# Performance work log

Hardware: AMD Instinct MI355X
Metric: run time of the kernel (lower is better)

The kernel has to match this reference:

```python
import jax, jax.numpy as jnp
import numpy as np

B, L, D, NLAYERS, MAX_NODES, DEG = 32, 512, 768, 3, 128, 8


def _build_graph():
    rng = np.random.default_rng(0)
    per = rng.integers(-32, 33, size=B // 2)
    sizes = np.concatenate([96 + per, 96 - per]).astype(np.int64)  # sum = 96*B = 3072, each in [64,128]
    N = int(sizes.sum())
    offs = np.concatenate([[0], np.cumsum(sizes)])
    batch = np.repeat(np.arange(B), sizes).astype(np.int64)
    pad_idx = np.zeros((B, MAX_NODES), np.int64)
    pad_mask = np.zeros((B, MAX_NODES), bool)
    src, dst = [], []
    for b in range(B):
        n = int(sizes[b])
        pad_idx[b, :n] = np.arange(offs[b], offs[b] + n)
        pad_mask[b, :n] = True
        src.append(rng.integers(offs[b], offs[b] + n, n * DEG))
        dst.append(rng.integers(offs[b], offs[b] + n, n * DEG))
    return N, batch, pad_idx, pad_mask, np.concatenate(src), np.concatenate(dst)


def setup_inputs() -> dict:
    N, batch, pad_idx, pad_mask, esrc, edst = _build_graph()
    key = jax.random.key(0)
    ks = jax.random.split(key, 8)
    s = 1.0 / np.sqrt(D)
    return {
        "x": jax.random.normal(ks[0], (N, D), jnp.float32),
        "text": jax.random.normal(ks[1], (B, L, D), jnp.float32),
        "batch_ent1_d_mask": jnp.ones((B, 1), jnp.float32),
        "batch_ent1_g_mask": jnp.ones((B, 1), jnp.float32),
        "gnn_ws": jax.random.normal(ks[2], (NLAYERS, D, D), jnp.float32) * s,
        "gnn_wn": jax.random.normal(ks[3], (NLAYERS, D, D), jnp.float32) * s,
        "gnn_b": jnp.zeros((NLAYERS, D), jnp.float32),
        "atom_w": jax.random.normal(ks[4], (D, D), jnp.float32) * s,
        "atom_b": jnp.zeros((D,), jnp.float32),
        "rand_emb": jax.random.normal(ks[5], (1, D), jnp.float32),
        "batch": jnp.asarray(batch),
        "pad_idx": jnp.asarray(pad_idx),
        "pad_mask": jnp.asarray(pad_mask),
        "edge_src": jnp.asarray(esrc),
        "edge_dst": jnp.asarray(edst),
    }


def reference(x, text, batch_ent1_d_mask, batch_ent1_g_mask, gnn_ws, gnn_wn, gnn_b,
              atom_w, atom_b, rand_emb, batch, pad_idx, pad_mask, edge_src, edge_dst):
    N = x.shape[0]
    E = edge_src.shape[0]
    maskf = pad_mask.astype(x.dtype)            # [B, M]
    n_per = maskf.sum(axis=1)                   # [B] num real nodes per graph
    # edge-neighbor mean counts (constants w.r.t. x)
    cnt = jax.ops.segment_sum(jnp.ones((E,), x.dtype), edge_dst, num_segments=N)
    inv_cnt = 1.0 / jnp.maximum(cnt, 1.0)
    cms = []
    for i in range(NLAYERS):
        # MoleGraphConv stand-in: mean neighbor aggregation + self transform
        msg = jax.ops.segment_sum(x[edge_src], edge_dst, num_segments=N) * inv_cnt[:, None]
        x = jax.nn.relu(x @ gnn_ws[i] + msg @ gnn_wn[i] + gnn_b[i])
        # ragged gather into padded [B, M, D]
        xp = x[pad_idx] * maskf[..., None]
        # graph -> text cross attention (softmax over text tokens; no mask needed)
        g2t = jax.nn.softmax(jnp.einsum('bmd,bld->bml', xp, text), axis=-1)
        g2t_out = jnp.einsum('bml,bld->bmd', g2t, text)            # [B, M, D]
        # text -> graph cross attention (mask padded nodes)
        t2g_logits = jnp.einsum('bld,bmd->blm', text, xp)
        t2g_logits = jnp.where(pad_mask[:, None, :], t2g_logits, jnp.float32(-1e9))
        t2g = jax.nn.softmax(t2g_logits, axis=-1)
        t2g_out = jnp.einsum('blm,bmd->bld', t2g, xp)              # [B, L, D]
        # mean over concatenated rows [n_i + L] per graph (pool_type=2)
        pooled = ((g2t_out * maskf[..., None]).sum(axis=1) + t2g_out.sum(axis=1)) \
                 / (n_per + jnp.float32(L))[:, None]
        cms.append(pooled)
    out_cms = jnp.mean(jnp.stack(cms, axis=1), axis=1)              # mean over layers
    out_t = text[:, 0, :]
    # scatter-mean of final node features per graph
    gsum = jax.ops.segment_sum(x, batch, num_segments=B)
    gcnt = jax.ops.segment_sum(jnp.ones((N,), x.dtype), batch, num_segments=B)
    xg = gsum / jnp.maximum(gcnt, 1.0)[:, None]
    # dropout is a no-op in eval mode
    out_g = jnp.tanh(xg @ atom_w + atom_b)
    z = rand_emb[0]
    dg = batch_ent1_d_mask * batch_ent1_g_mask
    return jnp.concatenate([
        out_t * batch_ent1_d_mask + (1 - batch_ent1_d_mask) * z,
        out_g * batch_ent1_g_mask + (1 - batch_ent1_g_mask) * z,
        out_cms * dg + (1 - dg) * z,
    ], axis=-1)
```

## Files before the change

kernel.cpp:

```cpp
#include <hip/hip_runtime.h>

#define D 768
#define B 32
#define L 512
#define M 128
#define NNODES 3072
#define NEDGES 24576

using bf16x8 = __attribute__((ext_vector_type(8))) short;
using f32x4  = __attribute__((ext_vector_type(4))) float;

__device__ __forceinline__ float bf2f(unsigned short u) {
  union { unsigned int i; float f; } v; v.i = ((unsigned int)u) << 16; return v.f;
}
__device__ __forceinline__ unsigned short f2bf(float f) {
  union { float f; unsigned int i; } v; v.f = f;
  unsigned int x = v.i;
  return (unsigned short)((x + 0x7FFFu + ((x >> 16) & 1u)) >> 16);
}
__device__ __forceinline__ float ldf(const void* p, size_t i, int f32) {
  return f32 ? ((const float*)p)[i] : bf2f(((const unsigned short*)p)[i]);
}
__device__ __forceinline__ int ldi(const void* p, size_t i, int w64) {
  return w64 ? (int)((const long long*)p)[i] : ((const int*)p)[i];
}
__device__ __forceinline__ f32x4 mfma16(bf16x8 a, bf16x8 b, f32x4 c) {
  return __builtin_amdgcn_mfma_f32_16x16x32_bf16(a, b, c, 0, 0, 0);
}
__device__ __forceinline__ void gl_lds(const unsigned short* gsrc, unsigned short* lbase,
                                       int lane) {
  __builtin_amdgcn_global_load_lds(
      (const __attribute__((address_space(1))) unsigned int*)(gsrc + lane * 8),
      (__attribute__((address_space(3))) unsigned int*)lbase, 16, 0, 0);
}

__device__ __forceinline__ float pk_read(const unsigned short* P, int p, int l, int d) {
  return bf2f(P[(((size_t)(p * 24 + (d >> 5))) << 9) + ((((d & 31) >> 3) << 4) + l) * 8 + (d & 7)]);
}

__device__ __forceinline__ void fma8(float* acc, float w, uint4 v) {
  unsigned xs[4] = {v.x, v.y, v.z, v.w};
#pragma unroll
  for (int j = 0; j < 4; ++j) {
    acc[2 * j]     += w * bf2f((unsigned short)(xs[j] & 0xFFFFu));
    acc[2 * j + 1] += w * bf2f((unsigned short)(xs[j] >> 16));
  }
}

__device__ __forceinline__ void acc12(float* a, const uint2* u) {
#pragma unroll
  for (int j = 0; j < 3; ++j) {
    a[j * 4 + 0] += bf2f((unsigned short)(u[j].x & 0xFFFFu));
    a[j * 4 + 1] += bf2f((unsigned short)(u[j].x >> 16));
    a[j * 4 + 2] += bf2f((unsigned short)(u[j].y & 0xFFFFu));
    a[j * 4 + 3] += bf2f((unsigned short)(u[j].y >> 16));
  }
}


__device__ void d_pack_in(const void* src, unsigned short* rows, unsigned short* dst,
                          int p, int tid, int f) {
  unsigned short* pb = dst + (size_t)p * 12288;
#pragma unroll
  for (int j = 0; j < 6; ++j) {
    int odx = j * 256 + tid;
    int kk = odx >> 6, lanep = odx & 63;
    int q = lanep >> 4, r16 = lanep & 15;
    int row = p * 16 + r16, col0 = kk * 32 + q * 8;
    size_t sbase = (size_t)row * 768 + col0;
    union { unsigned short v[8]; uint4 qv; } u;
    if (f) {
      const float* sp = (const float*)src + sbase;
      float4 v0 = *(const float4*)sp;
      float4 v1 = *(const float4*)(sp + 4);
      u.v[0] = f2bf(v0.x); u.v[1] = f2bf(v0.y); u.v[2] = f2bf(v0.z); u.v[3] = f2bf(v0.w);
      u.v[4] = f2bf(v1.x); u.v[5] = f2bf(v1.y); u.v[6] = f2bf(v1.z); u.v[7] = f2bf(v1.w);
    } else {
      u.qv = *(const uint4*)((const unsigned short*)src + sbase);
    }
    if (rows) *(uint4*)&rows[sbase] = u.qv;
    *(uint4*)&pb[(size_t)odx * 8] = u.qv;
  }
}

__device__ void d_pack(const unsigned short* src, unsigned short* dst,
                       int p, int tid) {
  unsigned short* pb = dst + (size_t)p * 12288;
#pragma unroll
  for (int j = 0; j < 6; ++j) {
    int odx = j * 256 + tid;
    int kk = odx >> 6, lanep = odx & 63;
    int q = lanep >> 4, r16 = lanep & 15;
    size_t sbase = (size_t)(p * 16 + r16) * 768 + kk * 32 + q * 8;
    uint4 qv = *(const uint4*)(src + sbase);
    *(uint4*)&pb[(size_t)odx * 8] = qv;
  }
}

__device__ void d_wpack(const void* Ws, const void* Wn, const void* Aw, int f,
                        unsigned short* WsPk, unsigned short* WnPk, unsigned short* AwPk,
                        int r0, int tid) {
  int z = r0 / 288, rem = r0 % 288;
  int nblk = rem % 12, kk = rem / 12;
  const void* src; unsigned short* dst; size_t zoff;
  if (z < 3)      { src = Ws; zoff = (size_t)z * D * D;       dst = WsPk + zoff; }
  else if (z < 6) { src = Wn; zoff = (size_t)(z - 3) * D * D; dst = WnPk + zoff; }
  else            { src = Aw; zoff = 0;                       dst = AwPk; }
  int pl = tid >> 6, lane = tid & 63;
  int pG = nblk * 4 + pl;
  int k0 = kk * 32 + ((lane >> 4) << 3);
  int n  = nblk * 64 + pl * 16 + (lane & 15);
  union { unsigned short v[8]; uint4 q; } u;
  if (f) {
    const float* sp = (const float*)src + zoff + (size_t)k0 * D + n;
#pragma unroll
    for (int e = 0; e < 8; ++e) u.v[e] = f2bf(sp[(size_t)e * D]);
  } else {
    const unsigned short* sp = (const unsigned short*)src + zoff + (size_t)k0 * D + n;
#pragma unroll
    for (int e = 0; e < 8; ++e) u.v[e] = sp[(size_t)e * D];
  }
  *(uint4*)&dst[(((size_t)(pG * 24 + kk)) << 9) + lane * 8] = u.q;
}

__device__ void d_count(const void* edst, const void* batch, int w,
                        int* cnt, int* gcnt, int i) {
  if (i < NEDGES) atomicAdd(&cnt[ldi(edst, i, w)], 1);
  if (i < NNODES) {
    int b = ldi(batch, i, w);
    int lane = i & 63;
    int prev = __shfl_up(b, 1);
    bool first = (lane == 0) || (prev != b);
    unsigned long long bm = __ballot(first ? 1 : 0);
    if (first) {
      unsigned long long higher = (lane < 63) ? (bm >> (lane + 1)) : 0ULL;
      int next = higher ? (lane + __ffsll((long long)higher)) : 64;
      atomicAdd(&gcnt[b], next - lane);
    }
  }
}

__device__ void d_msg(const unsigned short* x, const int* cnt, const int* rowstart,
                      const int* csr, unsigned short* Mpk, int p, int tid) {
  int w = tid >> 6, lane = tid & 63;
  unsigned short* pb = Mpk + (size_t)p * 12288;
#pragma unroll
  for (int i = 0; i < 4; i += 2) {
    int rA = w * 4 + i, rB = rA + 1;
    int nA = p * 16 + rA, nB = p * 16 + rB;
    int degA = cnt[nA], baseA = rowstart[nA];
    int degB = cnt[nB], baseB = rowstart[nB];
    float aA[12], aB[12];
#pragma unroll
    for (int j = 0; j < 12; ++j) { aA[j] = 0.f; aB[j] = 0.f; }
    int dmax = degA > degB ? degA : degB;
    for (int e = 0; e < dmax; ++e) {
      uint2 uA[3], uB[3];
      if (e < degA) {
        const uint2* xr = (const uint2*)(x + (size_t)csr[baseA + e] * D);
        uA[0] = xr[lane]; uA[1] = xr[lane + 64]; uA[2] = xr[lane + 128];
      }
      if (e < degB) {
        const uint2* xr = (const uint2*)(x + (size_t)csr[baseB + e] * D);
        uB[0] = xr[lane]; uB[1] = xr[lane + 64]; uB[2] = xr[lane + 128];
      }
      if (e < degA) acc12(aA, uA);
      if (e < degB) acc12(aB, uB);
    }
    float invA = 1.0f / (float)(degA > 1 ? degA : 1);
    float invB = 1.0f / (float)(degB > 1 ? degB : 1);
#pragma unroll
    for (int j = 0; j < 3; ++j) {
      int d0 = (lane + j * 64) * 4;
      int kk = d0 >> 5, q = (d0 >> 3) & 3, e0 = d0 & 7;
      uint2 wA, wB;
      wA.x = (unsigned int)f2bf(aA[j * 4 + 0] * invA)
           | ((unsigned int)f2bf(aA[j * 4 + 1] * invA) << 16);
      wA.y = (unsigned int)f2bf(aA[j * 4 + 2] * invA)
           | ((unsigned int)f2bf(aA[j * 4 + 3] * invA) << 16);
      wB.x = (unsigned int)f2bf(aB[j * 4 + 0] * invB)
           | ((unsigned int)f2bf(aB[j * 4 + 1] * invB) << 16);
      wB.y = (unsigned int)f2bf(aB[j * 4 + 2] * invB)
           | ((unsigned int)f2bf(aB[j * 4 + 3] * invB) << 16);
      *(uint2*)&pb[kk * 512 + (q * 16 + rA) * 8 + e0] = wA;
      *(uint2*)&pb[kk * 512 + (q * 16 + rB) * 8 + e0] = wB;
    }
  }
}

__device__ void d_gemm(const unsigned short* Xpk, const unsigned short* Mpk,
                       const unsigned short* WsPk, const unsigned short* WnPk,
                       const void* bias, size_t bias_off, int f,
                       unsigned short* Y, int bx, int by, int tid, char* smem) {
  unsigned short* lds = (unsigned short*)smem;
  int wave = tid >> 6, lane = tid & 63;
  int q = lane >> 4, t = lane & 15;
  int wm = wave >> 1, wn = wave & 1;
  int pa = bx * 4, pb = by * 4;
  f32x4 acc[2][2];
#pragma unroll
  for (int mi = 0; mi < 2; ++mi)
#pragma unroll
    for (int ni = 0; ni < 2; ++ni)
      acc[mi][ni] = (f32x4){0.f, 0.f, 0.f, 0.f};
  int c0 = wave * 2;
  int pan0 = (wave < 2) ? (pa + c0) : (pb + c0 - 4);
  auto issue = [&](int s) {
    int h = (s >= 24) ? 1 : 0;
    const unsigned short* P = (wave < 2) ? (h ? Mpk : Xpk) : (h ? WnPk : WsPk);
    int kk = s - h * 24;
    unsigned short* dbuf = &lds[(s & 3) * 4096 + c0 * 512];
    gl_lds(P + (((size_t)(pan0 * 24 + kk)) << 9), dbuf, lane);
    gl_lds(P + (((size_t)((pan0 + 1) * 24 + kk)) << 9), dbuf + 512, lane);
  };
  issue(0); issue(1); issue(2);
  for (int r = 0; r < 48; ++r) {
    if (r < 46)       asm volatile("s_waitcnt vmcnt(4)" ::: "memory");
    else if (r == 46) asm volatile("s_waitcnt vmcnt(2)" ::: "memory");
    else              asm volatile("s_waitcnt vmcnt(0)" ::: "memory");
    __builtin_amdgcn_s_barrier();
    asm volatile("" ::: "memory");
    if (r + 3 < 48) issue(r + 3);
    const unsigned short* bs = &lds[(r & 3) * 4096];
    bf16x8 a0 = *(const bf16x8*)&bs[(wm * 2 + 0) * 512 + lane * 8];
    bf16x8 a1 = *(const bf16x8*)&bs[(wm * 2 + 1) * 512 + lane * 8];
    bf16x8 b0 = *(const bf16x8*)&bs[(4 + wn * 2 + 0) * 512 + lane * 8];
    bf16x8 b1 = *(const bf16x8*)&bs[(4 + wn * 2 + 1) * 512 + lane * 8];
    acc[0][0] = mfma16(a0, b0, acc[0][0]);
    acc[0][1] = mfma16(a0, b1, acc[0][1]);
    acc[1][0] = mfma16(a1, b0, acc[1][0]);
    acc[1][1] = mfma16(a1, b1, acc[1][1]);
    asm volatile("" ::: "memory");
  }
#pragma unroll
  for (int ni = 0; ni < 2; ++ni) {
    int col = by * 64 + wn * 32 + ni * 16 + t;
    float bv = ldf(bias, bias_off + col, f);
#pragma unroll
    for (int mi = 0; mi < 2; ++mi) {
#pragma unroll
      for (int r = 0; r < 4; ++r) {
        int row = bx * 64 + wm * 32 + mi * 16 + q * 4 + r;
        float v = acc[mi][ni][r] + bv;
        Y[(size_t)row * D + col] = f2bf(v > 0.f ? v : 0.f);
      }
    }
  }
}

__device__ void d_xp(const unsigned short* Xn, const void* pidx, int w64,
                     const int* gcnt, unsigned short* xp, unsigned short* XpPk,
                     float* xgacc, int p, int tid, char* smem) {
  unsigned short* rows = (unsigned short*)smem;
  int r = tid >> 4, c16 = tid & 15;
  int bm = p * 16 + r;
  int b = bm >> 7, m = bm & 127;
  int nb = gcnt[b];
  uint4* dl = (uint4*)&rows[r * 776];
  uint4 v[6];
  if (m < nb) {
    const uint4* srcr = (const uint4*)(Xn + (size_t)ldi(pidx, bm, w64) * D);
#pragma unroll
    for (int j = 0; j < 6; ++j) v[j] = srcr[c16 + j * 16];
  } else {
    uint4 z = {0u, 0u, 0u, 0u};
#pragma unroll
    for (int j = 0; j < 6; ++j) v[j] = z;
  }
#pragma unroll
  for (int j = 0; j < 6; ++j) dl[c16 + j * 16] = v[j];
  __syncthreads();
#pragma unroll
  for (int j = 0; j < 6; ++j) {
    int idx = j * 256 + tid;
    int rr = idx / 96, cc = idx % 96;
    uint4 vv = *(const uint4*)&rows[rr * 776 + cc * 8];
    *(uint4*)&xp[(size_t)(p * 16 + rr) * D + cc * 8] = vv;
  }
  unsigned short* pb = XpPk + (size_t)p * 12288;
#pragma unroll
  for (int j = 0; j < 6; ++j) {
    int odx = j * 256 + tid;
    int kk = odx >> 6, lanep = odx & 63;
    int rr = lanep & 15, cg = lanep >> 4;
    int cc = kk * 4 + cg;
    uint4 vv = *(const uint4*)&rows[rr * 776 + cc * 8];
    *(uint4*)&pb[odx * 8] = vv;
  }
  if (xgacc) {
    int bb = p >> 3;
#pragma unroll
    for (int j = 0; j < 3; ++j) {
      int d = j * 256 + tid;
      float s = 0.f;
#pragma unroll
      for (int rr = 0; rr < 16; ++rr) s += bf2f(rows[rr * 776 + d]);
      atomicAdd(&xgacc[(size_t)bb * D + d], s);
    }
  }
}

__device__ void d_scores(const unsigned short* XpPk, const unsigned short* Tpk,
                         float* S, int bx, int by, int bz, int tid, char* smem) {
  unsigned short* lds = (unsigned short*)smem;
  int wave = tid >> 6, lane = tid & 63;
  int q = lane >> 4, t = lane & 15;
  int wm = wave >> 1, wn = wave & 1;
  int pa = bz * 8 + bx * 4;
  int pb = bz * 32 + by * 4;
  f32x4 acc[2][2];
#pragma unroll
  for (int mi = 0; mi < 2; ++mi)
#pragma unroll
    for (int ni = 0; ni < 2; ++ni)
      acc[mi][ni] = (f32x4){0.f, 0.f, 0.f, 0.f};
  int c0 = wave * 2;
  const unsigned short* P = (wave < 2) ? XpPk : Tpk;
  int pan0 = (wave < 2) ? (pa + c0) : (pb + c0 - 4);
  auto issue = [&](int kk) {
    unsigned short* dbuf = &lds[(kk & 3) * 4096 + c0 * 512];
    gl_lds(P + (((size_t)(pan0 * 24 + kk)) << 9), dbuf, lane);
    gl_lds(P + (((size_t)((pan0 + 1) * 24 + kk)) << 9), dbuf + 512, lane);
  };
  issue(0); issue(1); issue(2);
  for (int r = 0; r < 24; ++r) {
    if (r < 22)       asm volatile("s_waitcnt vmcnt(4)" ::: "memory");
    else if (r == 22) asm volatile("s_waitcnt vmcnt(2)" ::: "memory");
    else              asm volatile("s_waitcnt vmcnt(0)" ::: "memory");
    __builtin_amdgcn_s_barrier();
    asm volatile("" ::: "memory");
    if (r + 3 < 24) issue(r + 3);
    const unsigned short* bs = &lds[(r & 3) * 4096];
    bf16x8 a0 = *(const bf16x8*)&bs[(wm * 2 + 0) * 512 + lane * 8];
    bf16x8 a1 = *(const bf16x8*)&bs[(wm * 2 + 1) * 512 + lane * 8];
    bf16x8 b0 = *(const bf16x8*)&bs[(4 + wn * 2 + 0) * 512 + lane * 8];
    bf16x8 b1 = *(const bf16x8*)&bs[(4 + wn * 2 + 1) * 512 + lane * 8];
    acc[0][0] = mfma16(a0, b0, acc[0][0]);
    acc[0][1] = mfma16(a0, b1, acc[0][1]);
    acc[1][0] = mfma16(a1, b0, acc[1][0]);
    acc[1][1] = mfma16(a1, b1, acc[1][1]);
    asm volatile("" ::: "memory");
  }
  float* Sb = S + (size_t)bz * M * L;
#pragma unroll
  for (int ni = 0; ni < 2; ++ni) {
    int col = by * 64 + wn * 32 + ni * 16 + t;
#pragma unroll
    for (int mi = 0; mi < 2; ++mi) {
#pragma unroll
      for (int r = 0; r < 4; ++r) {
        int row = bx * 64 + wm * 32 + mi * 16 + q * 4 + r;
        Sb[(size_t)row * L + col] = acc[mi][ni][r];
      }
    }
  }
}

__device__ void d_stats(const float* S, const int* gcnt, float* rmax, float* rsum,
                        float* cmaxv, float* csumv, int bid, int tid, char* smem) {
  if (bid < B * M) {
    float* red = (float*)smem;
    int lane = tid & 63, wv = tid >> 6;
    const float* r = S + (size_t)bid * L;
    float s0 = r[tid], s1 = r[tid + 256];
    float m = fmaxf(s0, s1);
#pragma unroll
    for (int o = 32; o > 0; o >>= 1) m = fmaxf(m, __shfl_down(m, o));
    if (lane == 0) red[wv] = m;
    __syncthreads();
    float bm = fmaxf(fmaxf(red[0], red[1]), fmaxf(red[2], red[3]));
    __syncthreads();
    float e = __expf(s0 - bm) + __expf(s1 - bm);
#pragma unroll
    for (int o = 32; o > 0; o >>= 1) e += __shfl_down(e, o);
    if (lane == 0) red[wv] = e;
    __syncthreads();
    if (tid == 0) { rmax[bid] = bm; rsum[bid] = red[0] + red[1] + red[2] + red[3]; }
  } else {
    float (*pm)[64] = (float(*)[64])smem;
    float (*ps)[64] = (float(*)[64])(smem + 1024);
    int cid = bid - B * M;
    int b = cid >> 3, ly = cid & 7;
    int w = tid >> 6, lane = tid & 63;
    int l = ly * 64 + lane;
    int nb = gcnt[b];
    const float* Sb = S + (size_t)b * M * L;
    int m0 = w * 32, m1 = min(m0 + 32, nb);
    float cm = -1e30f, cs = 0.f;
    for (int m = m0; m < m1; ++m) {
      float s = Sb[(size_t)m * L + l];
      if (s > cm) { cs = cs * __expf(cm - s) + 1.f; cm = s; }
      else cs += __expf(s - cm);
    }
    pm[w][lane] = cm; ps[w][lane] = cs;
    __syncthreads();
    if (w == 0) {
      float CM = -1e30f;
#pragma unroll
      for (int j = 0; j < 4; ++j) CM = fmaxf(CM, pm[j][lane]);
      float CS = 0.f;
#pragma unroll
      for (int j = 0; j < 4; ++j) CS += ps[j][lane] * __expf(pm[j][lane] - CM);
      cmaxv[b * L + l] = CM; csumv[b * L + l] = CS;
    }
  }
}

__device__ void d_cross(const float* S, const float* rmax, const float* rsum,
                        const float* cmaxv, const float* csumv, const int* gcnt,
                        float* wv, float* t2gcol, int bid, int tid, char* smem) {
  if (bid < 256) {
    float* rm = (float*)smem;
    float* ri = (float*)(smem + 512);
    float (*pw)[64] = (float(*)[64])(smem + 1024);
    int b = bid >> 3, ly = bid & 7;
    int w = tid >> 6, lane = tid & 63;
    if (tid < M) { rm[tid] = rmax[b * M + tid]; ri[tid] = 1.f / rsum[b * M + tid]; }
    __syncthreads();
    int l = ly * 64 + lane;
    int nb = gcnt[b];
    const float* Sb = S + (size_t)b * M * L;
    int m0 = w * 32, m1 = min(m0 + 32, nb);
    float wp = 0.f;
    for (int m = m0; m < m1; ++m)
      wp += __expf(Sb[(size_t)m * L + l] - rm[m]) * ri[m];
    pw[w][lane] = wp;
    __syncthreads();
    if (w == 0)
      wv[b * L + l] = pw[0][lane] + pw[1][lane] + pw[2][lane] + pw[3][lane];
  } else {
    float* red = (float*)smem;
    int bm = bid - 256;
    int b = bm >> 7, m = bm & 127;
    int lane = tid & 63, w = tid >> 6;
    int nb = gcnt[b];
    float acc = 0.f;
    if (m < nb) {
      const float* r = S + (size_t)bm * L;
      const float* cm = cmaxv + b * L;
      const float* cs = csumv + b * L;
      acc = __expf(r[tid] - cm[tid]) / cs[tid]
          + __expf(r[tid + 256] - cm[tid + 256]) / cs[tid + 256];
    }
#pragma unroll
    for (int o = 32; o > 0; o >>= 1) acc += __shfl_down(acc, o);
    if (lane == 0) red[w] = acc;
    __syncthreads();
    if (tid == 0) t2gcol[bm] = red[0] + red[1] + red[2] + red[3];
  }
}

__device__ void d_pooled(const float* wv, const float* t2gcol, const unsigned short* Tpk,
                         const unsigned short* xp, const int* gcnt, float* pooled,
                         int bid, int tid, char* smem) {
  float* lred = (float*)smem;
  float* wbuf = (float*)(smem + 3072);
  int b = bid / 10, seg = bid - b * 10;
  int chunk = tid % 96, half = tid / 96;
  int d = chunk * 8;
  float acc[8];
#pragma unroll
  for (int j = 0; j < 8; ++j) acc[j] = 0.f;
  if (tid < 64) {
    wbuf[tid] = (seg < 8) ? wv[b * L + seg * 64 + tid]
                          : t2gcol[b * M + (seg - 8) * 64 + tid];
  }
  __syncthreads();
  if (half < 2) {
    if (seg < 8) {
      int pbase = b * 32 + seg * 4;
      size_t cbase = ((size_t)(d >> 5)) << 9;
      int coff = ((d & 31) >> 3) << 4;
      for (int i = 0; i < 32; ++i) {
        int l = half * 32 + i;
        const unsigned short* src =
            Tpk + (((size_t)((pbase + (l >> 4)) * 24)) << 9) + cbase +
            (size_t)(coff + (l & 15)) * 8;
        fma8(acc, wbuf[l], *(const uint4*)src);
      }
    } else {
      const unsigned short* Xb = xp + (size_t)b * M * D + d;
      int m0 = (seg - 8) * 64;
      for (int i = 0; i < 32; ++i) {
        int mm = half * 32 + i;
        fma8(acc, wbuf[mm], *(const uint4*)&Xb[(size_t)(m0 + mm) * D]);
      }
    }
  }
  if (half == 1) {
#pragma unroll
    for (int j = 0; j < 8; ++j) lred[chunk * 8 + j] = acc[j];
  }
  __syncthreads();
  if (half == 0) {
    float inv = 1.f / ((float)gcnt[b] + 512.f);
#pragma unroll
    for (int j = 0; j < 8; ++j)
      atomicAdd(&pooled[(size_t)b * D + d + j], (acc[j] + lred[chunk * 8 + j]) * inv);
  }
}

__device__ void d_atom(const float* xgacc, const int* gcnt, const unsigned short* AwPk,
                       float* gpre, int bid, int tid) {
  int w = tid >> 6, lane = tid & 63;
  int q = lane >> 4, t = lane & 15;
  int nbase = bid * 64 + w * 16;
  int pb = nbase >> 4;
  int n0 = gcnt[t], n1 = gcnt[16 + t];
  float inv0 = 1.f / (float)(n0 > 1 ? n0 : 1);
  float inv1 = 1.f / (float)(n1 > 1 ? n1 : 1);
  f32x4 acc[2];
  acc[0] = (f32x4){0.f, 0.f, 0.f, 0.f};
  acc[1] = (f32x4){0.f, 0.f, 0.f, 0.f};
  for (int kk = 0; kk < 24; ++kk) {
    const float* s0 = xgacc + (size_t)t * D + kk * 32 + q * 8;
    const float* s1 = xgacc + (size_t)(16 + t) * D + kk * 32 + q * 8;
    union { unsigned short v[8]; bf16x8 f; } a0, a1;
#pragma unroll
    for (int j = 0; j < 8; ++j) { a0.v[j] = f2bf(s0[j] * inv0); a1.v[j] = f2bf(s1[j] * inv1); }
    bf16x8 bv = *(const bf16x8*)(AwPk + (((size_t)(pb * 24 + kk)) << 9) + (lane << 3));
    acc[0] = mfma16(a0.f, bv, acc[0]);
    acc[1] = mfma16(a1.f, bv, acc[1]);
  }
#pragma unroll
  for (int mi = 0; mi < 2; ++mi)
#pragma unroll
    for (int r = 0; r < 4; ++r) {
      int row = mi * 16 + q * 4 + r;
      gpre[(size_t)row * D + nbase + t] = acc[mi][r];
    }
}


__global__ void k_init(int* cnt, int* cursor, int* gcnt, float* pooled, float* xgacc,
                       const unsigned short* __restrict__ t,
                       const unsigned int* __restrict__ e, int* __restrict__ flags) {
  int i = blockIdx.x * 256 + threadIdx.x;
  if (i < NNODES) { cnt[i] = 0; cursor[i] = 0; }
  if (i < B) gcnt[i] = 0;
  if (i < B * D) { pooled[i] = 0.f; xgacc[i] = 0.f; }
  if (blockIdx.x == 0) {
    __shared__ int r0[256];
    __shared__ unsigned r1[256];
    int tid = threadIdx.x;
    int bad = 0;
    for (int j = tid; j < 8192; j += 256) {
      unsigned short u = t[2 * j];
      unsigned ex = (u >> 7) & 0xFF;
      if (ex >= 0xC0) bad = 1;
    }
    unsigned o = 0;
    for (int j = tid; j < NEDGES / 2; j += 256) o |= e[2 * j + 1];
    r0[tid] = bad; r1[tid] = o;
    __syncthreads();
    for (int s = 128; s > 0; s >>= 1) {
      if (tid < s) { r0[tid] |= r0[tid + s]; r1[tid] |= r1[tid + s]; }
      __syncthreads();
    }
    if (tid == 0) { flags[0] = r0[0]; flags[1] = (r1[0] == 0) ? 1 : 0; }
  }
}

__global__ __launch_bounds__(256) void k_setup2(
    const void* x_in, unsigned short* x0, unsigned short* PkA,
    const void* text, unsigned short* Tpk,
    const void* Ws, const void* Wn, const void* Aw,
    unsigned short* WsPk, unsigned short* WnPk, unsigned short* AwPk,
    const void* edst, const void* batch, int* cnt, int* gcnt,
    const int* __restrict__ flags) {
  int bid = blockIdx.x, tid = threadIdx.x;
  if (bid < 1216) {
    int f = flags[0];
    if (bid < NNODES / 16) d_pack_in(x_in, x0, PkA, bid, tid, f);
    else d_pack_in(text, nullptr, Tpk, bid - NNODES / 16, tid, f);
  } else if (bid < 3232) {
    d_wpack(Ws, Wn, Aw, flags[0], WsPk, WnPk, AwPk, bid - 1216, tid);
  } else {
    d_count(edst, batch, flags[1], cnt, gcnt, (bid - 3232) * 256 + tid);
  }
}

__global__ void k_scan(const int* __restrict__ cnt, int* __restrict__ rowstart) {
  __shared__ int a[NNODES], b[NNODES];
  int tid = threadIdx.x;
  for (int i = tid; i < NNODES; i += 1024) a[i] = cnt[i];
  __syncthreads();
  int* s = a; int* d = b;
  for (int off = 1; off < NNODES; off <<= 1) {
    for (int i = tid; i < NNODES; i += 1024)
      d[i] = s[i] + (i >= off ? s[i - off] : 0);
    __syncthreads();
    int* t = s; s = d; d = t;
  }
  for (int i = tid; i < NNODES; i += 1024) rowstart[i + 1] = s[i];
  if (tid == 0) rowstart[0] = 0;
}

__global__ void k_scatter(const void* __restrict__ esrc, const void* __restrict__ edst,
                          const int* __restrict__ flags, const int* __restrict__ rowstart,
                          int* __restrict__ cursor, int* __restrict__ csr) {
  int w = flags[1];
  int i = blockIdx.x * 256 + threadIdx.x;
  if (i < NEDGES) {
    int dd = ldi(edst, i, w);
    int pos = atomicAdd(&cursor[dd], 1);
    csr[rowstart[dd] + pos] = ldi(esrc, i, w);
  }
}

__global__ __launch_bounds__(256) void k_msgp(
    const unsigned short* x, const int* cnt, const int* rowstart, const int* csr,
    unsigned short* Mpk) {
  d_msg(x, cnt, rowstart, csr, Mpk, blockIdx.x, threadIdx.x);
}

__device__ __forceinline__ void gemm_map(int g, int& bx, int& by) {
  int gs = (g % 8) * 72 + g / 8;
  bx = gs / 12; by = gs % 12;
}
__device__ __forceinline__ void sc_map(int g, int& bx, int& by, int& bz) {
  int gs = (g % 8) * 64 + g / 8;
  bx = gs & 1; by = (gs >> 1) & 7; bz = gs >> 4;
}

__global__ __launch_bounds__(256) void k_gemm(
    const unsigned short* Apk, const unsigned short* Mpk,
    const unsigned short* WsPk, const unsigned short* WnPk,
    const void* bias, unsigned long bias_off, const int* flags, unsigned short* Y) {
  extern __shared__ char smem[];
  int bx, by; gemm_map(blockIdx.x, bx, by);
  d_gemm(Apk, Mpk, WsPk, WnPk, bias, bias_off, flags[0], Y, bx, by,
         threadIdx.x, smem);
}

__global__ __launch_bounds__(256) void k_postg(
    const unsigned short* Y, unsigned short* Npk, int packN,
    const void* pidx, const int* flags, const int* gcnt,
    unsigned short* xp, unsigned short* XpPk, float* xgacc) {
  extern __shared__ char smem[];
  int bid = blockIdx.x, tid = threadIdx.x;
  if (bid < packN) d_pack(Y, Npk, bid, tid);
  else d_xp(Y, pidx, flags[1], gcnt, xp, XpPk, xgacc, bid - packN, tid, smem);
}

__global__ __launch_bounds__(256) void k_scmsg(
    const unsigned short* XpPk, const unsigned short* Tpk, float* S,
    int msgN, const unsigned short* x, const int* cnt, const int* rowstart,
    const int* csr, unsigned short* Mpk) {
  extern __shared__ char smem[];
  int bid = blockIdx.x, tid = threadIdx.x;
  if (bid < 512) {
    int bx, by, bz; sc_map(bid, bx, by, bz);
    d_scores(XpPk, Tpk, S, bx, by, bz, tid, smem);
  } else d_msg(x, cnt, rowstart, csr, Mpk, bid - 512, tid);
}

__global__ __launch_bounds__(256) void k_stgemm(
    const float* S, const int* gcnt, float* rmax, float* rsum, float* cmaxv, float* csumv,
    int gemmN, const unsigned short* Apk, const unsigned short* Mpk,
    const unsigned short* WsPk, const unsigned short* WnPk,
    const void* bias, unsigned long bias_off, const int* flags, unsigned short* Y) {
  extern __shared__ char smem[];
  int bid = blockIdx.x, tid = threadIdx.x;
  if (bid < 4352) d_stats(S, gcnt, rmax, rsum, cmaxv, csumv, bid, tid, smem);
  else {
    int bx, by; gemm_map(bid - 4352, bx, by);
    d_gemm(Apk, Mpk, WsPk, WnPk, bias, bias_off, flags[0], Y, bx, by, tid, smem);
  }
}

__global__ __launch_bounds__(256) void k_crpostg(
    const float* S, const float* rmax, const float* rsum, const float* cmaxv,
    const float* csumv, const int* gcnt, float* wv, float* t2gcol,
    int packN, int xpN, const unsigned short* Y, unsigned short* Npk,
    const void* pidx, const int* flags, unsigned short* xp, unsigned short* XpPk,
    float* xgacc) {
  extern __shared__ char smem[];
  int bid = blockIdx.x, tid = threadIdx.x;
  if (bid < 4352) d_cross(S, rmax, rsum, cmaxv, csumv, gcnt, wv, t2gcol, bid, tid, smem);
  else {
    int r = bid - 4352;
    if (r < packN) d_pack(Y, Npk, r, tid);
    else d_xp(Y, pidx, flags[1], gcnt, xp, XpPk, xgacc, r - packN, tid, smem);
  }
}

__global__ __launch_bounds__(256) void k_plscmsg(
    const float* wv, const float* t2gcol, const unsigned short* Tpk,
    const unsigned short* xpL, const int* gcnt, float* pooled,
    int scN, const unsigned short* XpPk, float* S,
    int msgN, const unsigned short* x, const int* cnt, const int* rowstart,
    const int* csr, unsigned short* Mpk,
    int atomN, const float* xgacc, const unsigned short* AwPk, float* gpre) {
  extern __shared__ char smem[];
  int bid = blockIdx.x, tid = threadIdx.x;
  if (bid < 320) { d_pooled(wv, t2gcol, Tpk, xpL, gcnt, pooled, bid, tid, smem); return; }
  int r = bid - 320;
  if (r < scN) {
    int bx, by, bz; sc_map(r, bx, by, bz);
    d_scores(XpPk, Tpk, S, bx, by, bz, tid, smem); return;
  }
  r -= scN;
  if (r < msgN) { d_msg(x, cnt, rowstart, csr, Mpk, r, tid); return; }
  d_atom(xgacc, gcnt, AwPk, gpre, r - msgN, tid);
}

__global__ __launch_bounds__(256) void k_final(
    const unsigned short* __restrict__ Tpk, const float* __restrict__ gpre,
    const float* __restrict__ pooled, const void* __restrict__ ab,
    const void* __restrict__ dmask, const void* __restrict__ gmask,
    const void* __restrict__ remb, const int* __restrict__ flags,
    void* __restrict__ out) {
  int f = flags[0];
  int b = blockIdx.x, tid = threadIdx.x;
  float dm = ldf(dmask, b, f);
  float gm = ldf(gmask, b, f);
  float dg = dm * gm;
  size_t base = (size_t)b * 2304;
#pragma unroll
  for (int j = 0; j < 3; ++j) {
    int d = tid + j * 256;
    float z = ldf(remb, d, f);
    float tv = pk_read(Tpk, b * 32, 0, d);
    float o0 = tv * dm + (1.f - dm) * z;
    float gv = tanhf(gpre[(size_t)b * D + d] + ldf(ab, d, f));
    float o1 = gv * gm + (1.f - gm) * z;
    float p = pooled[(size_t)b * D + d] * (1.f / 3.f);
    float o2 = p * dg + (1.f - dg) * z;
    if (f) {
      float* of = (float*)out;
      of[base + d] = o0; of[base + 768 + d] = o1; of[base + 1536 + d] = o2;
    } else {
      unsigned short* ob = (unsigned short*)out;
      ob[base + d] = f2bf(o0); ob[base + 768 + d] = f2bf(o1); ob[base + 1536 + d] = f2bf(o2);
    }
  }
}

extern "C" void kernel_launch(void* const* d_in, const int* in_sizes, int n_in,
                              void* d_out, int out_size, void* d_ws, size_t ws_size,
                              hipStream_t stream) {
  const void* x_in  = d_in[0];
  const void* text  = d_in[1];
  const void* dmask = d_in[2];
  const void* gmask = d_in[3];
  const void* gws   = d_in[4];
  const void* gwn   = d_in[5];
  const void* gb    = d_in[6];
  const void* aw    = d_in[7];
  const void* ab    = d_in[8];
  const void* remb  = d_in[9];
  const void* batch = d_in[10];
  const void* pidx  = d_in[11];
  const void* esrc  = d_in[13];
  const void* edst  = d_in[14];

  char* wsp = (char*)d_ws;
  size_t off = 0;
  auto carve = [&](size_t bytes) -> void* {
    void* p = wsp + off;
    off += (bytes + 255) & ~(size_t)255;
    return p;
  };
  int* flags = (int*)carve(2 * 4);
  unsigned short* x0    = (unsigned short*)carve((size_t)NNODES * D * 2);
  unsigned short* xA    = (unsigned short*)carve((size_t)NNODES * D * 2);
  unsigned short* xB    = (unsigned short*)carve((size_t)NNODES * D * 2);
  unsigned short* PkA   = (unsigned short*)carve((size_t)NNODES * D * 2);
  unsigned short* PkB   = (unsigned short*)carve((size_t)NNODES * D * 2);
  unsigned short* Mpk   = (unsigned short*)carve((size_t)NNODES * D * 2);
  unsigned short* Tpk   = (unsigned short*)carve((size_t)B * L * D * 2);
  unsigned short* WsPk  = (unsigned short*)carve((size_t)3 * D * D * 2);
  unsigned short* WnPk  = (unsigned short*)carve((size_t)3 * D * D * 2);
  unsigned short* AwPk  = (unsigned short*)carve((size_t)D * D * 2);
  unsigned short* xpA   = (unsigned short*)carve((size_t)B * M * D * 2);
  unsigned short* xpB   = (unsigned short*)carve((size_t)B * M * D * 2);
  unsigned short* XpPkA = (unsigned short*)carve((size_t)B * M * D * 2);
  unsigned short* XpPkB = (unsigned short*)carve((size_t)B * M * D * 2);
  float* xgacc   = (float*)carve((size_t)B * D * 4);
  float* gpre    = (float*)carve((size_t)B * D * 4);
  float* S       = (float*)carve((size_t)B * M * L * 4);
  float* rmax    = (float*)carve((size_t)B * M * 4);
  float* rsum    = (float*)carve((size_t)B * M * 4);
  float* wv      = (float*)carve((size_t)B * L * 4);
  float* cmaxv   = (float*)carve((size_t)B * L * 4);
  float* csumv   = (float*)carve((size_t)B * L * 4);
  float* t2gcol  = (float*)carve((size_t)B * M * 4);
  float* pooled  = (float*)carve((size_t)B * D * 4);
  int* cnt      = (int*)carve((size_t)NNODES * 4);
  int* rowstart = (int*)carve((size_t)(NNODES + 1) * 4);
  int* cursor   = (int*)carve((size_t)NNODES * 4);
  int* gcnt     = (int*)carve((size_t)B * 4);
  int* csr      = (int*)carve((size_t)NEDGES * 4);

  const size_t DD = (size_t)D * D;

  k_init<<<96, 256, 0, stream>>>(cnt, cursor, gcnt, pooled, xgacc,
                                 (const unsigned short*)text, (const unsigned int*)edst, flags);
  k_setup2<<<3328, 256, 0, stream>>>(x_in, x0, PkA, text, Tpk, gws, gwn, aw,
                                     WsPk, WnPk, AwPk, edst, batch, cnt, gcnt, flags);
  k_scan<<<1, 1024, 0, stream>>>(cnt, rowstart);
  k_scatter<<<96, 256, 0, stream>>>(esrc, edst, flags, rowstart, cursor, csr);

  k_msgp<<<192, 256, 0, stream>>>(x0, cnt, rowstart, csr, Mpk);
  k_gemm<<<576, 256, 32768, stream>>>(PkA, Mpk, WsPk, WnPk, gb, 0, flags, xA);
  k_postg<<<448, 256, 24832, stream>>>(xA, PkB, 192, pidx, flags, gcnt, xpA, XpPkA, nullptr);
  k_scmsg<<<704, 256, 32768, stream>>>(XpPkA, Tpk, S, 192, xA, cnt, rowstart, csr, Mpk);
  k_stgemm<<<4928, 256, 32768, stream>>>(S, gcnt, rmax, rsum, cmaxv, csumv,
                                         576, PkB, Mpk, WsPk + DD, WnPk + DD, gb, D, flags, xB);
  k_crpostg<<<4800, 256, 24832, stream>>>(S, rmax, rsum, cmaxv, csumv, gcnt, wv, t2gcol,
                                          192, 256, xB, PkA, pidx, flags, xpB, XpPkB, nullptr);
  k_plscmsg<<<1024, 256, 32768, stream>>>(wv, t2gcol, Tpk, xpA, gcnt, pooled,
                                          512, XpPkB, S, 192, xB, cnt, rowstart, csr, Mpk,
                                          0, nullptr, nullptr, nullptr);
  k_stgemm<<<4928, 256, 32768, stream>>>(S, gcnt, rmax, rsum, cmaxv, csumv,
                                         576, PkA, Mpk, WsPk + 2 * DD, WnPk + 2 * DD,
                                         gb, 2 * D, flags, xA);
  k_crpostg<<<4608, 256, 24832, stream>>>(S, rmax, rsum, cmaxv, csumv, gcnt, wv, t2gcol,
                                          0, 256, xA, nullptr, pidx, flags, xpA, XpPkA, xgacc);
  k_plscmsg<<<832, 256, 32768, stream>>>(wv, t2gcol, Tpk, xpB, gcnt, pooled,
                                         512, XpPkA, S, 0, nullptr, nullptr, nullptr,
                                         nullptr, nullptr, 0, nullptr, nullptr, nullptr);
  k_stgemm<<<4352, 256, 2048, stream>>>(S, gcnt, rmax, rsum, cmaxv, csumv,
                                        0, nullptr, nullptr, nullptr, nullptr,
                                        nullptr, 0, flags, nullptr);
  k_crpostg<<<4352, 256, 2048, stream>>>(S, rmax, rsum, cmaxv, csumv, gcnt, wv, t2gcol,
                                         0, 0, nullptr, nullptr, pidx, flags,
                                         nullptr, nullptr, nullptr);
  k_plscmsg<<<332, 256, 4096, stream>>>(wv, t2gcol, Tpk, xpA, gcnt, pooled,
                                        0, nullptr, nullptr, 0, nullptr, nullptr, nullptr,
                                        nullptr, nullptr, 12, xgacc, AwPk, gpre);
  k_final<<<32, 256, 0, stream>>>(Tpk, gpre, pooled, ab, dmask, gmask, remb, flags, d_out);
}
```

Before: 463.0 us.

## Load GEMM and score operands directly from global memory instead of LDS staging

The GEMM and attention-score tiles now load their bf16 MFMA operands straight from global memory into registers, with each wave reading its own panels. This drops the global-to-LDS asynchronous staging ring, the block barriers and the explicit waitcnt pipeline. Dynamic shared memory for the affected launches shrinks from 32 KB to 0, 2 KB or 4 KB, which frees LDS and could raise occupancy. The cost is that panels once shared across waves through LDS are now fetched redundantly per wave, and load latency is hidden only by unrolling and wave switching rather than explicit prefetch.

```diff
diff --git a/kernel.cpp b/kernel.cpp
--- a/kernel.cpp
+++ b/kernel.cpp
@@ -26,12 +26,6 @@
 }
 __device__ __forceinline__ f32x4 mfma16(bf16x8 a, bf16x8 b, f32x4 c) {
   return __builtin_amdgcn_mfma_f32_16x16x32_bf16(a, b, c, 0, 0, 0);
-}
-__device__ __forceinline__ void gl_lds(const unsigned short* gsrc, unsigned short* lbase,
-                                       int lane) {
-  __builtin_amdgcn_global_load_lds(
-      (const __attribute__((address_space(1))) unsigned int*)(gsrc + lane * 8),
-      (__attribute__((address_space(3))) unsigned int*)lbase, 16, 0, 0);
 }
 
 __device__ __forceinline__ float pk_read(const unsigned short* P, int p, int l, int d) {
@@ -191,46 +185,48 @@
 __device__ void d_gemm(const unsigned short* Xpk, const unsigned short* Mpk,
                        const unsigned short* WsPk, const unsigned short* WnPk,
                        const void* bias, size_t bias_off, int f,
-                       unsigned short* Y, int bx, int by, int tid, char* smem) {
-  unsigned short* lds = (unsigned short*)smem;
+                       unsigned short* Y, int bx, int by, int tid) {
   int wave = tid >> 6, lane = tid & 63;
   int q = lane >> 4, t = lane & 15;
   int wm = wave >> 1, wn = wave & 1;
-  int pa = bx * 4, pb = by * 4;
+  const int PAN = 24 << 9;
   f32x4 acc[2][2];
 #pragma unroll
   for (int mi = 0; mi < 2; ++mi)
 #pragma unroll
     for (int ni = 0; ni < 2; ++ni)
       acc[mi][ni] = (f32x4){0.f, 0.f, 0.f, 0.f};
-  int c0 = wave * 2;
-  int pan0 = (wave < 2) ? (pa + c0) : (pb + c0 - 4);
-  auto issue = [&](int s) {
-    int h = (s >= 24) ? 1 : 0;
-    const unsigned short* P = (wave < 2) ? (h ? Mpk : Xpk) : (h ? WnPk : WsPk);
-    int kk = s - h * 24;
-    unsigned short* dbuf = &lds[(s & 3) * 4096 + c0 * 512];
-    gl_lds(P + (((size_t)(pan0 * 24 + kk)) << 9), dbuf, lane);
-    gl_lds(P + (((size_t)((pan0 + 1) * 24 + kk)) << 9), dbuf + 512, lane);
-  };
-  issue(0); issue(1); issue(2);
-  for (int r = 0; r < 48; ++r) {
-    if (r < 46)       asm volatile("s_waitcnt vmcnt(4)" ::: "memory");
-    else if (r == 46) asm volatile("s_waitcnt vmcnt(2)" ::: "memory");
-    else              asm volatile("s_waitcnt vmcnt(0)" ::: "memory");
-    __builtin_amdgcn_s_barrier();
-    asm volatile("" ::: "memory");
-    if (r + 3 < 48) issue(r + 3);
-    const unsigned short* bs = &lds[(r & 3) * 4096];
-    bf16x8 a0 = *(const bf16x8*)&bs[(wm * 2 + 0) * 512 + lane * 8];
-    bf16x8 a1 = *(const bf16x8*)&bs[(wm * 2 + 1) * 512 + lane * 8];
-    bf16x8 b0 = *(const bf16x8*)&bs[(4 + wn * 2 + 0) * 512 + lane * 8];
-    bf16x8 b1 = *(const bf16x8*)&bs[(4 + wn * 2 + 1) * 512 + lane * 8];
-    acc[0][0] = mfma16(a0, b0, acc[0][0]);
-    acc[0][1] = mfma16(a0, b1, acc[0][1]);
-    acc[1][0] = mfma16(a1, b0, acc[1][0]);
-    acc[1][1] = mfma16(a1, b1, acc[1][1]);
-    asm volatile("" ::: "memory");
+  size_t aoff = (((size_t)((bx * 4 + wm * 2) * 24)) << 9) + lane * 8;
+  size_t boff = (((size_t)((by * 4 + wn * 2) * 24)) << 9) + lane * 8;
+  {
+    const unsigned short* A = Xpk + aoff;
+    const unsigned short* Bp = WsPk + boff;
+#pragma unroll 4
+    for (int kk = 0; kk < 24; ++kk) {
+      bf16x8 a0 = *(const bf16x8*)(A + kk * 512);
+      bf16x8 a1 = *(const bf16x8*)(A + kk * 512 + PAN);
+      bf16x8 b0 = *(const bf16x8*)(Bp + kk * 512);
+      bf16x8 b1 = *(const bf16x8*)(Bp + kk * 512 + PAN);
+      acc[0][0] = mfma16(a0, b0, acc[0][0]);
+      acc[0][1] = mfma16(a0, b1, acc[0][1]);
+      acc[1][0] = mfma16(a1, b0, acc[1][0]);
+      acc[1][1] = mfma16(a1, b1, acc[1][1]);
+    }
+  }
+  {
+    const unsigned short* A = Mpk + aoff;
+    const unsigned short* Bp = WnPk + boff;
+#pragma unroll 4
+    for (int kk = 0; kk < 24; ++kk) {
+      bf16x8 a0 = *(const bf16x8*)(A + kk * 512);
+      bf16x8 a1 = *(const bf16x8*)(A + kk * 512 + PAN);
+      bf16x8 b0 = *(const bf16x8*)(Bp + kk * 512);
+      bf16x8 b1 = *(const bf16x8*)(Bp + kk * 512 + PAN);
+      acc[0][0] = mfma16(a0, b0, acc[0][0]);
+      acc[0][1] = mfma16(a0, b1, acc[0][1]);
+      acc[1][0] = mfma16(a1, b0, acc[1][0]);
+      acc[1][1] = mfma16(a1, b1, acc[1][1]);
+    }
   }
 #pragma unroll
   for (int ni = 0; ni < 2; ++ni) {
@@ -301,45 +297,31 @@
 }
 
 __device__ void d_scores(const unsigned short* XpPk, const unsigned short* Tpk,
-                         float* S, int bx, int by, int bz, int tid, char* smem) {
-  unsigned short* lds = (unsigned short*)smem;
+                         float* S, int bx, int by, int bz, int tid) {
   int wave = tid >> 6, lane = tid & 63;
   int q = lane >> 4, t = lane & 15;
   int wm = wave >> 1, wn = wave & 1;
-  int pa = bz * 8 + bx * 4;
-  int pb = bz * 32 + by * 4;
+  const int PAN = 24 << 9;
   f32x4 acc[2][2];
 #pragma unroll
   for (int mi = 0; mi < 2; ++mi)
 #pragma unroll
     for (int ni = 0; ni < 2; ++ni)
       acc[mi][ni] = (f32x4){0.f, 0.f, 0.f, 0.f};
-  int c0 = wave * 2;
-  const unsigned short* P = (wave < 2) ? XpPk : Tpk;
-  int pan0 = (wave < 2) ? (pa + c0) : (pb + c0 - 4);
-  auto issue = [&](int kk) {
-    unsigned short* dbuf = &lds[(kk & 3) * 4096 + c0 * 512];
-    gl_lds(P + (((size_t)(pan0 * 24 + kk)) << 9), dbuf, lane);
-    gl_lds(P + (((size_t)((pan0 + 1) * 24 + kk)) << 9), dbuf + 512, lane);
-  };
-  issue(0); issue(1); issue(2);
-  for (int r = 0; r < 24; ++r) {
-    if (r < 22)       asm volatile("s_waitcnt vmcnt(4)" ::: "memory");
-    else if (r == 22) asm volatile("s_waitcnt vmcnt(2)" ::: "memory");
-    else              asm volatile("s_waitcnt vmcnt(0)" ::: "memory");
-    __builtin_amdgcn_s_barrier();
-    asm volatile("" ::: "memory");
-    if (r + 3 < 24) issue(r + 3);
-    const unsigned short* bs = &lds[(r & 3) * 4096];
-    bf16x8 a0 = *(const bf16x8*)&bs[(wm * 2 + 0) * 512 + lane * 8];
-    bf16x8 a1 = *(const bf16x8*)&bs[(wm * 2 + 1) * 512 + lane * 8];
-    bf16x8 b0 = *(const bf16x8*)&bs[(4 + wn * 2 + 0) * 512 + lane * 8];
-    bf16x8 b1 = *(const bf16x8*)&bs[(4 + wn * 2 + 1) * 512 + lane * 8];
+  size_t aoff = (((size_t)((bz * 8 + bx * 4 + wm * 2) * 24)) << 9) + lane * 8;
+  size_t boff = (((size_t)((bz * 32 + by * 4 + wn * 2) * 24)) << 9) + lane * 8;
+  const unsigned short* A = XpPk + aoff;
+  const unsigned short* Bp = Tpk + boff;
+#pragma unroll 4
+  for (int kk = 0; kk < 24; ++kk) {
+    bf16x8 a0 = *(const bf16x8*)(A + kk * 512);
+    bf16x8 a1 = *(const bf16x8*)(A + kk * 512 + PAN);
+    bf16x8 b0 = *(const bf16x8*)(Bp + kk * 512);
+    bf16x8 b1 = *(const bf16x8*)(Bp + kk * 512 + PAN);
     acc[0][0] = mfma16(a0, b0, acc[0][0]);
     acc[0][1] = mfma16(a0, b1, acc[0][1]);
     acc[1][0] = mfma16(a1, b0, acc[1][0]);
     acc[1][1] = mfma16(a1, b1, acc[1][1]);
-    asm volatile("" ::: "memory");
   }
   float* Sb = S + (size_t)bz * M * L;
 #pragma unroll
@@ -627,10 +609,8 @@
     const unsigned short* Apk, const unsigned short* Mpk,
     const unsigned short* WsPk, const unsigned short* WnPk,
     const void* bias, unsigned long bias_off, const int* flags, unsigned short* Y) {
-  extern __shared__ char smem[];
   int bx, by; gemm_map(blockIdx.x, bx, by);
-  d_gemm(Apk, Mpk, WsPk, WnPk, bias, bias_off, flags[0], Y, bx, by,
-         threadIdx.x, smem);
+  d_gemm(Apk, Mpk, WsPk, WnPk, bias, bias_off, flags[0], Y, bx, by, threadIdx.x);
 }
 
 __global__ __launch_bounds__(256) void k_postg(
@@ -647,11 +627,10 @@
     const unsigned short* XpPk, const unsigned short* Tpk, float* S,
     int msgN, const unsigned short* x, const int* cnt, const int* rowstart,
     const int* csr, unsigned short* Mpk) {
-  extern __shared__ char smem[];
   int bid = blockIdx.x, tid = threadIdx.x;
   if (bid < 512) {
     int bx, by, bz; sc_map(bid, bx, by, bz);
-    d_scores(XpPk, Tpk, S, bx, by, bz, tid, smem);
+    d_scores(XpPk, Tpk, S, bx, by, bz, tid);
   } else d_msg(x, cnt, rowstart, csr, Mpk, bid - 512, tid);
 }
 
@@ -665,7 +644,7 @@
   if (bid < 4352) d_stats(S, gcnt, rmax, rsum, cmaxv, csumv, bid, tid, smem);
   else {
     int bx, by; gemm_map(bid - 4352, bx, by);
-    d_gemm(Apk, Mpk, WsPk, WnPk, bias, bias_off, flags[0], Y, bx, by, tid, smem);
+    d_gemm(Apk, Mpk, WsPk, WnPk, bias, bias_off, flags[0], Y, bx, by, tid);
   }
 }
 
@@ -698,7 +677,7 @@
   int r = bid - 320;
   if (r < scN) {
     int bx, by, bz; sc_map(r, bx, by, bz);
-    d_scores(XpPk, Tpk, S, bx, by, bz, tid, smem); return;
+    d_scores(XpPk, Tpk, S, bx, by, bz, tid); return;
   }
   r -= scN;
   if (r < msgN) { d_msg(x, cnt, rowstart, csr, Mpk, r, tid); return; }
@@ -803,24 +782,24 @@
   k_scatter<<<96, 256, 0, stream>>>(esrc, edst, flags, rowstart, cursor, csr);
 
   k_msgp<<<192, 256, 0, stream>>>(x0, cnt, rowstart, csr, Mpk);
-  k_gemm<<<576, 256, 32768, stream>>>(PkA, Mpk, WsPk, WnPk, gb, 0, flags, xA);
+  k_gemm<<<576, 256, 0, stream>>>(PkA, Mpk, WsPk, WnPk, gb, 0, flags, xA);
   k_postg<<<448, 256, 24832, stream>>>(xA, PkB, 192, pidx, flags, gcnt, xpA, XpPkA, nullptr);
-  k_scmsg<<<704, 256, 32768, stream>>>(XpPkA, Tpk, S, 192, xA, cnt, rowstart, csr, Mpk);
-  k_stgemm<<<4928, 256, 32768, stream>>>(S, gcnt, rmax, rsum, cmaxv, csumv,
-                                         576, PkB, Mpk, WsPk + DD, WnPk + DD, gb, D, flags, xB);
+  k_scmsg<<<704, 256, 0, stream>>>(XpPkA, Tpk, S, 192, xA, cnt, rowstart, csr, Mpk);
+  k_stgemm<<<4928, 256, 2048, stream>>>(S, gcnt, rmax, rsum, cmaxv, csumv,
+                                        576, PkB, Mpk, WsPk + DD, WnPk + DD, gb, D, flags, xB);
   k_crpostg<<<4800, 256, 24832, stream>>>(S, rmax, rsum, cmaxv, csumv, gcnt, wv, t2gcol,
                                           192, 256, xB, PkA, pidx, flags, xpB, XpPkB, nullptr);
-  k_plscmsg<<<1024, 256, 32768, stream>>>(wv, t2gcol, Tpk, xpA, gcnt, pooled,
-                                          512, XpPkB, S, 192, xB, cnt, rowstart, csr, Mpk,
-                                          0, nullptr, nullptr, nullptr);
-  k_stgemm<<<4928, 256, 32768, stream>>>(S, gcnt, rmax, rsum, cmaxv, csumv,
-                                         576, PkA, Mpk, WsPk + 2 * DD, WnPk + 2 * DD,
-                                         gb, 2 * D, flags, xA);
+  k_plscmsg<<<1024, 256, 4096, stream>>>(wv, t2gcol, Tpk, xpA, gcnt, pooled,
+                                         512, XpPkB, S, 192, xB, cnt, rowstart, csr, Mpk,
+                                         0, nullptr, nullptr, nullptr);
+  k_stgemm<<<4928, 256, 2048, stream>>>(S, gcnt, rmax, rsum, cmaxv, csumv,
+                                        576, PkA, Mpk, WsPk + 2 * DD, WnPk + 2 * DD,
+                                        gb, 2 * D, flags, xA);
   k_crpostg<<<4608, 256, 24832, stream>>>(S, rmax, rsum, cmaxv, csumv, gcnt, wv, t2gcol,
                                           0, 256, xA, nullptr, pidx, flags, xpA, XpPkA, xgacc);
-  k_plscmsg<<<832, 256, 32768, stream>>>(wv, t2gcol, Tpk, xpB, gcnt, pooled,
-                                         512, XpPkA, S, 0, nullptr, nullptr, nullptr,
-                                         nullptr, nullptr, 0, nullptr, nullptr, nullptr);
+  k_plscmsg<<<832, 256, 4096, stream>>>(wv, t2gcol, Tpk, xpB, gcnt, pooled,
+                                        512, XpPkA, S, 0, nullptr, nullptr, nullptr,
+                                        nullptr, nullptr, 0, nullptr, nullptr, nullptr);
   k_stgemm<<<4352, 256, 2048, stream>>>(S, gcnt, rmax, rsum, cmaxv, csumv,
                                         0, nullptr, nullptr, nullptr, nullptr,
                                         nullptr, 0, flags, nullptr);
```

After: 421.2 us. -9.0%, faster.
